# Performance work log

Hardware: AMD Instinct MI355X
Metric: run time of the kernel (lower is better)

The kernel has to match this reference:

```python
import jax, jax.numpy as jnp
import numpy as np

N = 100_000      # nodes
E = 1_600_000    # edges (avg degree 16)
IN, H, OUT = 128, 64, 32
G = 128          # graphs in batch
EPS = 1e-5


def setup_inputs() -> dict:
    key = jax.random.key(0)
    ks = jax.random.split(key, 12)
    x = jax.random.normal(ks[0], (N, IN), jnp.float32)
    edge_index = jax.random.randint(ks[1], (2, E), 0, N, dtype=jnp.int32)
    batch = jnp.sort(jax.random.randint(ks[2], (N,), 0, G, dtype=jnp.int32))
    # GCNConv weights (glorot-ish scaling), shared BatchNorm params, final linear
    W1 = jax.random.normal(ks[3], (IN, H), jnp.float32) / np.sqrt(IN)
    b1 = jnp.zeros((H,), jnp.float32)
    W2 = jax.random.normal(ks[4], (H, H), jnp.float32) / np.sqrt(H)
    b2 = jnp.zeros((H,), jnp.float32)
    gamma = jnp.ones((H,), jnp.float32)
    beta = jnp.zeros((H,), jnp.float32)
    linW = jax.random.normal(ks[5], (H, OUT), jnp.float32) / np.sqrt(H)
    linb = jnp.zeros((OUT,), jnp.float32)
    return dict(x=x, edge_index=edge_index, batch=batch, W1=W1, b1=b1,
                W2=W2, b2=b2, gamma=gamma, beta=beta, linW=linW, linb=linb)


def _gcn_edges(edge_index):
    # add self loops (PyG GCNConv default) and symmetric normalization
    loop = jnp.arange(N, dtype=edge_index.dtype)
    src = jnp.concatenate([edge_index[0], loop])
    dst = jnp.concatenate([edge_index[1], loop])
    deg = jax.ops.segment_sum(jnp.ones_like(src, jnp.float32), dst, num_segments=N)
    dis = jnp.where(deg > 0, jax.lax.rsqrt(deg), 0.0)
    norm = dis[src] * dis[dst]          # [E+N]
    return src, dst, norm


def _gcn_conv(h, W, b, src, dst, norm):
    h = h @ W                            # [N, out] small GEMM first (PyG order)
    msg = h[src] * norm[:, None]         # gather + edgewise normalize
    return jax.ops.segment_sum(msg, dst, num_segments=N) + b  # scatter-add


def _batchnorm(h, gamma, beta):
    # training-mode batch stats over nodes (biased variance, as torch BN)
    mean = h.mean(axis=0)
    var = jnp.mean((h - mean) ** 2, axis=0)
    return (h - mean) * jax.lax.rsqrt(var + EPS) * gamma + beta


def reference(x, edge_index, batch, W1, b1, W2, b2, gamma, beta, linW, linb):
    src, dst, norm = _gcn_edges(edge_index)
    h = jax.nn.relu(_batchnorm(_gcn_conv(x, W1, b1, src, dst, norm), gamma, beta))
    h = jax.nn.relu(_batchnorm(_gcn_conv(h, W2, b2, src, dst, norm), gamma, beta))
    # global mean pool over graph ids
    sums = jax.ops.segment_sum(h, batch, num_segments=G)
    cnts = jax.ops.segment_sum(jnp.ones((N,), h.dtype), batch, num_segments=G)
    pooled = sums / jnp.maximum(cnts, 1.0)[:, None]   # [G, H]
    return pooled @ linW + linb                        # [G, OUT]
```

## Files before the change

### kernel.cpp

```cpp
#include <hip/hip_runtime.h>

#define NNODES 100000
#define NEDGES 1600000
#define FIN 128
#define FH 64
#define FOUT 32
#define NGRAPH 128
#define EPSV 1e-5f

#define SCAN_BT 256
#define NBLK ((NNODES + SCAN_BT - 1) / SCAN_BT)
#define GM ((NNODES + 63) / 64)
#define FILLBLK 2048

typedef unsigned short ushort_t;
typedef __attribute__((ext_vector_type(8))) short bf16x8;
typedef __attribute__((ext_vector_type(4))) float f32x4;

__device__ inline unsigned f2bf(float f) {
  union { float f; unsigned u; } x;
  x.f = f;
  return (x.u + 0x7fffu + ((x.u >> 16) & 1u)) >> 16;
}
__device__ inline unsigned pack2(float a, float b) { return f2bf(a) | (f2bf(b) << 16); }
__device__ inline float bflo(unsigned u) {
  union { unsigned u; float f; } x;
  x.u = u << 16;
  return x.f;
}
__device__ inline float bfhi(unsigned u) {
  union { unsigned u; float f; } x;
  x.u = u & 0xffff0000u;
  return x.f;
}
__device__ inline float bfone(ushort_t v) {
  union { unsigned u; float f; } x;
  x.u = ((unsigned)v) << 16;
  return x.f;
}


__global__ void k_deg_accum(const int* __restrict__ dst, int* __restrict__ deg) {
  const int SLICE = NNODES / 8;
  int xcd = blockIdx.x & 7;
  int lo = xcd * SLICE, hi = lo + SLICE;
  int chunk = blockIdx.x >> 3;
  int nchunk = gridDim.x >> 3;
  for (int i = chunk * blockDim.x + threadIdx.x; i < NEDGES; i += nchunk * blockDim.x) {
    int d = dst[i];
    if (d >= lo && d < hi) atomicAdd(&deg[d], 1);
  }
}


__global__ void k_blocksum(const int* __restrict__ deg, int* __restrict__ bsum) {
  __shared__ int ls[SCAN_BT];
  int b = blockIdx.x, t = threadIdx.x;
  int i = b * SCAN_BT + t;
  ls[t] = (i < NNODES) ? deg[i] : 0;
  __syncthreads();
  for (int s = SCAN_BT / 2; s > 0; s >>= 1) {
    if (t < s) ls[t] += ls[t + s];
    __syncthreads();
  }
  if (t == 0) bsum[b] = ls[0];
}

__global__ void k_scan_bsums(const int* __restrict__ bsum, int* __restrict__ boff) {
  __shared__ int ls[512];
  int t = threadIdx.x;
  int v = (t < NBLK) ? bsum[t] : 0;
  ls[t] = v;
  __syncthreads();
  for (int s = 1; s < 512; s <<= 1) {
    int add = (t >= s) ? ls[t - s] : 0;
    __syncthreads();
    ls[t] += add;
    __syncthreads();
  }
  if (t < NBLK) boff[t] = ls[t] - v;
}

__global__ void k_scan_final(const int* __restrict__ deg, const int* __restrict__ boff,
                             int* __restrict__ off, float* __restrict__ dis) {
  __shared__ int ls[SCAN_BT];
  int b = blockIdx.x, t = threadIdx.x;
  int i = b * SCAN_BT + t;
  int v = (i < NNODES) ? deg[i] : 0;
  ls[t] = v;
  __syncthreads();
  for (int s = 1; s < SCAN_BT; s <<= 1) {
    int add = (t >= s) ? ls[t - s] : 0;
    __syncthreads();
    ls[t] += add;
    __syncthreads();
  }
  if (i < NNODES) {
    off[i] = boff[b] + ls[t] - v;
    dis[i] = rsqrtf((float)v + 1.0f);
  }
  if (i == NNODES - 1) off[NNODES] = boff[b] + ls[t];
}


template <int K, bool BN>
__device__ __forceinline__ void gemm_body(int bid, const void* __restrict__ Ap,
                                          const float* __restrict__ W,
                                          const float* __restrict__ stats,
                                          const float* __restrict__ gamma,
                                          const float* __restrict__ beta,
                                          const float* __restrict__ dis,
                                          ushort_t* __restrict__ out) {
  const int WT = K + 8;
  __shared__ ushort_t wt[64 * (K + 8)];
  __shared__ float bn_sc[K], bn_sh[K];
  if (BN && threadIdx.x < K) {
    int f = threadIdx.x;
    float mean = stats[f] * (1.0f / NNODES);
    float var = stats[K + f] * (1.0f / NNODES) - mean * mean;
    float s = gamma[f] * rsqrtf(var + EPSV);
    bn_sc[f] = s;
    bn_sh[f] = beta[f] - mean * s;
  }
  for (int idx = threadIdx.x; idx < K * 64; idx += 256) {
    int k = idx >> 6, col = idx & 63;
    wt[col * WT + k] = (ushort_t)f2bf(W[idx]);
  }
  __syncthreads();

  int wave = threadIdx.x >> 6;
  int lane = threadIdx.x & 63;
  int rrow = lane & 15;
  int g = lane >> 4;
  int row0 = (bid * 4 + wave) * 16;
  int arow = min(row0 + rrow, NNODES - 1);

  f32x4 acc0 = {0.f, 0.f, 0.f, 0.f}, acc1 = acc0, acc2 = acc0, acc3 = acc0;

#pragma unroll
  for (int ks = 0; ks < K / 32; ++ks) {
    int koff = ks * 32 + g * 8;
    float xs[8];
    if (BN) {
      const ushort_t* a = (const ushort_t*)Ap + (long long)arow * K;
      uint4 ua = *(const uint4*)(a + koff);
      xs[0] = bflo(ua.x); xs[1] = bfhi(ua.x);
      xs[2] = bflo(ua.y); xs[3] = bfhi(ua.y);
      xs[4] = bflo(ua.z); xs[5] = bfhi(ua.z);
      xs[6] = bflo(ua.w); xs[7] = bfhi(ua.w);
#pragma unroll
      for (int j = 0; j < 8; ++j)
        xs[j] = fmaxf(fmaf(xs[j], bn_sc[koff + j], bn_sh[koff + j]), 0.0f);
    } else {
      const float* a = (const float*)Ap + (long long)arow * K;
      f32x4 xa = __builtin_nontemporal_load((const f32x4*)(a + koff));
      f32x4 xb = __builtin_nontemporal_load((const f32x4*)(a + koff + 4));
      xs[0] = xa.x; xs[1] = xa.y; xs[2] = xa.z; xs[3] = xa.w;
      xs[4] = xb.x; xs[5] = xb.y; xs[6] = xb.z; xs[7] = xb.w;
    }
    bf16x8 af;
#pragma unroll
    for (int j = 0; j < 8; ++j) af[j] = (short)f2bf(xs[j]);
    bf16x8 b0 = *(const bf16x8*)&wt[(0 * 16 + rrow) * WT + koff];
    bf16x8 b1 = *(const bf16x8*)&wt[(1 * 16 + rrow) * WT + koff];
    bf16x8 b2 = *(const bf16x8*)&wt[(2 * 16 + rrow) * WT + koff];
    bf16x8 b3 = *(const bf16x8*)&wt[(3 * 16 + rrow) * WT + koff];
    acc0 = __builtin_amdgcn_mfma_f32_16x16x32_bf16(af, b0, acc0, 0, 0, 0);
    acc1 = __builtin_amdgcn_mfma_f32_16x16x32_bf16(af, b1, acc1, 0, 0, 0);
    acc2 = __builtin_amdgcn_mfma_f32_16x16x32_bf16(af, b2, acc2, 0, 0, 0);
    acc3 = __builtin_amdgcn_mfma_f32_16x16x32_bf16(af, b3, acc3, 0, 0, 0);
  }

  int orow0 = row0 + g * 4;
#pragma unroll
  for (int r = 0; r < 4; ++r) {
    int orow = orow0 + r;
    if (orow < NNODES) {
      float d = dis[orow];
      ushort_t* o = out + (long long)orow * FH + rrow;
      o[0] = (ushort_t)f2bf(acc0[r] * d);
      o[16] = (ushort_t)f2bf(acc1[r] * d);
      o[32] = (ushort_t)f2bf(acc2[r] * d);
      o[48] = (ushort_t)f2bf(acc3[r] * d);
    }
  }
}

template <int K, bool BN>
__global__ void k_gemm_mfma(const void* __restrict__ A, const float* __restrict__ W,
                            const float* __restrict__ stats, const float* __restrict__ gamma,
                            const float* __restrict__ beta, const float* __restrict__ dis,
                            ushort_t* __restrict__ out) {
  gemm_body<K, BN>(blockIdx.x, A, W, stats, gamma, beta, dis, out);
}


__global__ void k_fill_gemm1(const float* __restrict__ x, const float* __restrict__ W1,
                             const float* __restrict__ dis, ushort_t* __restrict__ bufA,
                             const int* __restrict__ src, const int* __restrict__ dst,
                             const int* __restrict__ off, int* __restrict__ cursor,
                             int* __restrict__ csr) {
  if (blockIdx.x < GM) {
    gemm_body<FIN, false>(blockIdx.x, x, W1, nullptr, nullptr, nullptr, dis, bufA);
  } else {
    int bb = blockIdx.x - GM;
    const int SLICE = NNODES / 8;
    int xcd = bb & 7;
    int lo = xcd * SLICE, hi = lo + SLICE;
    int chunk = bb >> 3;
    int nchunk = FILLBLK >> 3;
    for (int i = chunk * blockDim.x + threadIdx.x; i < NEDGES; i += nchunk * blockDim.x) {
      int d = dst[i];
      if (d >= lo && d < hi) {
        int p = atomicAdd(&cursor[d], 1);
        csr[off[d] + p] = src[i];
      }
    }
  }
}


#define ACC8(acc, u, ok)                       \
  acc[0] += (ok) ? bflo(u.x) : 0.0f;           \
  acc[1] += (ok) ? bfhi(u.x) : 0.0f;           \
  acc[2] += (ok) ? bflo(u.y) : 0.0f;           \
  acc[3] += (ok) ? bfhi(u.y) : 0.0f;           \
  acc[4] += (ok) ? bflo(u.z) : 0.0f;           \
  acc[5] += (ok) ? bfhi(u.z) : 0.0f;           \
  acc[6] += (ok) ? bflo(u.w) : 0.0f;           \
  acc[7] += (ok) ? bfhi(u.w) : 0.0f;

__global__ void k_gather(const ushort_t* __restrict__ hs, const int* __restrict__ csr,
                         const int* __restrict__ off, const float* __restrict__ dis,
                         ushort_t* __restrict__ out, float* __restrict__ stats) {
  __shared__ float ls[2 * FH];
  int tid = threadIdx.x;
  if (tid < 2 * FH) ls[tid] = 0.0f;
  __syncthreads();
  int lane = tid & 63;
  int q = lane >> 3;
  int i = lane & 7;
  int wid = (blockIdx.x * blockDim.x + tid) >> 6;
  int nw = (gridDim.x * blockDim.x) >> 6;
  const int HALF = NNODES / 2;
  float s1[8], s2[8];
#pragma unroll
  for (int f = 0; f < 8; ++f) s1[f] = s2[f] = 0.0f;

  for (int p = wid; p < HALF; p += nw) {
    int dA = p, dB = p + HALF;
    int bA = off[dA], eA = off[dA + 1];
    int bB = off[dB], eB = off[dB + 1];
    uint4 selfA = *(const uint4*)(hs + (long long)dA * FH + i * 8);
    uint4 selfB = *(const uint4*)(hs + (long long)dB * FH + i * 8);
    float accA[8], accB[8];
#pragma unroll
    for (int f = 0; f < 8; ++f) accA[f] = accB[f] = 0.0f;
    bool q0 = (q == 0);
    ACC8(accA, selfA, q0);
    ACC8(accB, selfB, q0);

    int nA = (eA - bA + 15) >> 4, nB = (eB - bB + 15) >> 4;
    int niter = max(nA, nB);
    int lastA = max(eA - 1, 0), lastB = max(eB - 1, 0);
    int kA0 = bA + q, kA1 = bA + q + 8;
    int kB0 = bB + q, kB1 = bB + q + 8;
    for (int j = 0; j < niter; ++j) {
      int a0 = kA0 + 16 * j, a1 = kA1 + 16 * j;
      int b0 = kB0 + 16 * j, b1 = kB1 + 16 * j;
      int cA0 = csr[min(a0, lastA)];
      int cA1 = csr[min(a1, lastA)];
      int cB0 = csr[min(b0, lastB)];
      int cB1 = csr[min(b1, lastB)];
      uint4 uA0 = *(const uint4*)(hs + (long long)cA0 * FH + i * 8);
      uint4 uA1 = *(const uint4*)(hs + (long long)cA1 * FH + i * 8);
      uint4 uB0 = *(const uint4*)(hs + (long long)cB0 * FH + i * 8);
      uint4 uB1 = *(const uint4*)(hs + (long long)cB1 * FH + i * 8);
      bool A0 = a0 < eA, A1 = a1 < eA, B0 = b0 < eB, B1 = b1 < eB;
      ACC8(accA, uA0, A0);
      ACC8(accA, uA1, A1);
      ACC8(accB, uB0, B0);
      ACC8(accB, uB1, B1);
    }
#pragma unroll
    for (int f = 0; f < 8; ++f) {
      accA[f] += __shfl_xor(accA[f], 8);
      accA[f] += __shfl_xor(accA[f], 16);
      accA[f] += __shfl_xor(accA[f], 32);
      accB[f] += __shfl_xor(accB[f], 8);
      accB[f] += __shfl_xor(accB[f], 16);
      accB[f] += __shfl_xor(accB[f], 32);
    }
    float ddA = dis[dA], ddB = dis[dB];
#pragma unroll
    for (int f = 0; f < 8; ++f) {
      accA[f] *= ddA;
      accB[f] *= ddB;
      s1[f] += accA[f] + accB[f];
      s2[f] += accA[f] * accA[f] + accB[f] * accB[f];
    }
    if (q == 0) {
      uint4 o;
      o.x = pack2(accA[0], accA[1]);
      o.y = pack2(accA[2], accA[3]);
      o.z = pack2(accA[4], accA[5]);
      o.w = pack2(accA[6], accA[7]);
      *(uint4*)(out + (long long)dA * FH + i * 8) = o;
    } else if (q == 1) {
      uint4 o;
      o.x = pack2(accB[0], accB[1]);
      o.y = pack2(accB[2], accB[3]);
      o.z = pack2(accB[4], accB[5]);
      o.w = pack2(accB[6], accB[7]);
      *(uint4*)(out + (long long)dB * FH + i * 8) = o;
    }
  }
  if (q == 2) {
#pragma unroll
    for (int f = 0; f < 8; ++f) {
      atomicAdd(&ls[i * 8 + f], s1[f]);
      atomicAdd(&ls[FH + i * 8 + f], s2[f]);
    }
  }
  __syncthreads();
  if (tid < 2 * FH) atomicAdd(&stats[tid], ls[tid]);
}


#define POOL_WAVES 1024

__global__ void k_pool(const ushort_t* __restrict__ h, const int* __restrict__ batch,
                       const float* __restrict__ stats, const float* __restrict__ gamma,
                       const float* __restrict__ beta, float* __restrict__ pooled,
                       float* __restrict__ cnt) {
  const int CHUNK = (NNODES + POOL_WAVES - 1) / POOL_WAVES;
  int lane = threadIdx.x & 63;
  int wid = (blockIdx.x * blockDim.x + threadIdx.x) >> 6;
  int start = wid * CHUNK;
  if (start >= NNODES) return;
  int end = min(start + CHUNK, NNODES);
  float mean = stats[lane] * (1.0f / NNODES);
  float var = stats[FH + lane] * (1.0f / NNODES) - mean * mean;
  float sc = gamma[lane] * rsqrtf(var + EPSV);
  float sh = beta[lane] - mean * sc;
  int cur = batch[start];
  float acc = 0.0f;
  int cl = 0;
  for (int n = start; n < end; ++n) {
    int g = batch[n];
    if (g != cur) {
      atomicAdd(&pooled[cur * FH + lane], acc);
      if (lane == 0) atomicAdd(&cnt[cur], (float)cl);
      acc = 0.0f;
      cl = 0;
      cur = g;
    }
    float v = fmaf(bfone(h[(long long)n * FH + lane]), sc, sh);
    acc += fmaxf(v, 0.0f);
    ++cl;
  }
  atomicAdd(&pooled[cur * FH + lane], acc);
  if (lane == 0) atomicAdd(&cnt[cur], (float)cl);
}


__global__ void k_final(const float* __restrict__ pooled, const float* __restrict__ cnt,
                        const float* __restrict__ linW, const float* __restrict__ linb,
                        float* __restrict__ out) {
  int t = blockIdx.x * blockDim.x + threadIdx.x;
  if (t >= NGRAPH * FOUT) return;
  int g = t / FOUT, o = t % FOUT;
  float inv = 1.0f / fmaxf(cnt[g], 1.0f);
  float acc = linb[o];
#pragma unroll
  for (int k = 0; k < FH; ++k) acc = fmaf(pooled[g * FH + k] * inv, linW[k * FOUT + o], acc);
  out[t] = acc;
}

extern "C" void kernel_launch(void* const* d_in, const int* in_sizes, int n_in,
                              void* d_out, int out_size, void* d_ws, size_t ws_size,
                              hipStream_t stream) {
  const float* x = (const float*)d_in[0];
  const int* edge_index = (const int*)d_in[1];
  const int* batch = (const int*)d_in[2];
  const float* W1 = (const float*)d_in[3];
  const float* W2 = (const float*)d_in[5];
  const float* gamma = (const float*)d_in[7];
  const float* beta = (const float*)d_in[8];
  const float* linW = (const float*)d_in[9];
  const float* linb = (const float*)d_in[10];
  float* out = (float*)d_out;

  const int* esrc = edge_index;
  const int* edst = edge_index + NEDGES;

  ushort_t* bufA = (ushort_t*)d_ws;
  ushort_t* bufB = bufA + (long long)NNODES * FH;
  float* dis = (float*)(bufB + (long long)NNODES * FH);
  int* off = (int*)(dis + NNODES);
  int* csr = off + (NNODES + 1);
  int* bsum = csr + NEDGES;
  int* boff = bsum + NBLK;
  int* deg = boff + NBLK;
  int* cursor = deg + NNODES;
  float* stats1 = (float*)(cursor + NNODES);
  float* stats2 = stats1 + 2 * FH;
  float* pooled = stats2 + 2 * FH;
  float* cnt = pooled + NGRAPH * FH;

  const int BT = 256;

  hipMemsetAsync(deg, 0,
                 (size_t)(2 * NNODES + 2 * 2 * FH + NGRAPH * FH + NGRAPH) * sizeof(int), stream);

  k_deg_accum<<<2048, BT, 0, stream>>>(edst, deg);
  k_blocksum<<<NBLK, SCAN_BT, 0, stream>>>(deg, bsum);
  k_scan_bsums<<<1, 512, 0, stream>>>(bsum, boff);
  k_scan_final<<<NBLK, SCAN_BT, 0, stream>>>(deg, boff, off, dis);
  k_fill_gemm1<<<GM + FILLBLK, BT, 0, stream>>>(x, W1, dis, bufA, esrc, edst, off, cursor, csr);

  k_gather<<<2048, BT, 0, stream>>>(bufA, csr, off, dis, bufB, stats1);

  k_gemm_mfma<FH, true><<<GM, BT, 0, stream>>>(bufB, W2, stats1, gamma, beta, dis, bufA);
  k_gather<<<2048, BT, 0, stream>>>(bufA, csr, off, dis, bufB, stats2);

  k_pool<<<POOL_WAVES * 64 / BT, BT, 0, stream>>>(bufB, batch, stats2, gamma, beta, pooled, cnt);
  k_final<<<(NGRAPH * FOUT + BT - 1) / BT, BT, 0, stream>>>(pooled, cnt, linW, linb, out);
}
```

Before: 425.1 us.

## Fuse all GCN stages into one cooperative persistent kernel with grid syncs

```diff
diff --git a/kernel.cpp b/kernel.cpp
--- a/kernel.cpp
+++ b/kernel.cpp
@@ -1,4 +1,7 @@
 #include <hip/hip_runtime.h>
+#include <hip/hip_cooperative_groups.h>
+
+namespace cg = cooperative_groups;
 
 #define NNODES 100000
 #define NEDGES 1600000
@@ -8,10 +11,11 @@
 #define NGRAPH 128
 #define EPSV 1e-5f
 
-#define SCAN_BT 256
-#define NBLK ((NNODES + SCAN_BT - 1) / SCAN_BT)
+#define NBLK ((NNODES + 255) / 256)
 #define GM ((NNODES + 63) / 64)
+#define FILLITEMS 1024
 #define FILLBLK 2048
+#define POOL_WAVES 1024
 
 typedef unsigned short ushort_t;
 typedef __attribute__((ext_vector_type(8))) short bf16x8;
@@ -39,68 +43,32 @@
   return x.f;
 }
 
-
-__global__ void k_deg_accum(const int* __restrict__ dst, int* __restrict__ deg) {
-  const int SLICE = NNODES / 8;
-  int xcd = blockIdx.x & 7;
-  int lo = xcd * SLICE, hi = lo + SLICE;
-  int chunk = blockIdx.x >> 3;
-  int nchunk = gridDim.x >> 3;
-  for (int i = chunk * blockDim.x + threadIdx.x; i < NEDGES; i += nchunk * blockDim.x) {
-    int d = dst[i];
-    if (d >= lo && d < hi) atomicAdd(&deg[d], 1);
-  }
-}
-
-
-__global__ void k_blocksum(const int* __restrict__ deg, int* __restrict__ bsum) {
-  __shared__ int ls[SCAN_BT];
-  int b = blockIdx.x, t = threadIdx.x;
-  int i = b * SCAN_BT + t;
-  ls[t] = (i < NNODES) ? deg[i] : 0;
-  __syncthreads();
-  for (int s = SCAN_BT / 2; s > 0; s >>= 1) {
-    if (t < s) ls[t] += ls[t + s];
-    __syncthreads();
-  }
-  if (t == 0) bsum[b] = ls[0];
-}
-
-__global__ void k_scan_bsums(const int* __restrict__ bsum, int* __restrict__ boff) {
-  __shared__ int ls[512];
-  int t = threadIdx.x;
-  int v = (t < NBLK) ? bsum[t] : 0;
-  ls[t] = v;
-  __syncthreads();
-  for (int s = 1; s < 512; s <<= 1) {
-    int add = (t >= s) ? ls[t - s] : 0;
-    __syncthreads();
-    ls[t] += add;
-    __syncthreads();
-  }
-  if (t < NBLK) boff[t] = ls[t] - v;
-}
-
-__global__ void k_scan_final(const int* __restrict__ deg, const int* __restrict__ boff,
-                             int* __restrict__ off, float* __restrict__ dis) {
-  __shared__ int ls[SCAN_BT];
-  int b = blockIdx.x, t = threadIdx.x;
-  int i = b * SCAN_BT + t;
-  int v = (i < NNODES) ? deg[i] : 0;
-  ls[t] = v;
-  __syncthreads();
-  for (int s = 1; s < SCAN_BT; s <<= 1) {
-    int add = (t >= s) ? ls[t - s] : 0;
-    __syncthreads();
-    ls[t] += add;
-    __syncthreads();
-  }
-  if (i < NNODES) {
-    off[i] = boff[b] + ls[t] - v;
-    dis[i] = rsqrtf((float)v + 1.0f);
-  }
-  if (i == NNODES - 1) off[NNODES] = boff[b] + ls[t];
-}
+struct P {
+  const float* x;
+  const int* src;
+  const int* dst;
+  const int* batch;
+  const float* W1;
+  const float* W2;
+  const float* gamma;
+  const float* beta;
+  const float* linW;
+  const float* linb;
+  float* out;
+  ushort_t* bufA;
+  ushort_t* bufB;
+  float* dis;
+  int* off;
+  int* csr;
+  int* bsum;
+  int* boff;
+  int* deg;
+  int* cursor;
+  float* stats1;
+  float* stats2;
+  float* pooled;
+  float* cnt;
+};
 
 
 template <int K, bool BN>
@@ -110,10 +78,10 @@
                                           const float* __restrict__ gamma,
                                           const float* __restrict__ beta,
                                           const float* __restrict__ dis,
-                                          ushort_t* __restrict__ out) {
+                                          ushort_t* __restrict__ out, ushort_t* wt,
+                                          float* bn_sc, float* bn_sh) {
   const int WT = K + 8;
-  __shared__ ushort_t wt[64 * (K + 8)];
-  __shared__ float bn_sc[K], bn_sh[K];
+  __syncthreads();
   if (BN && threadIdx.x < K) {
     int f = threadIdx.x;
     float mean = stats[f] * (1.0f / NNODES);
@@ -186,39 +154,6 @@
   }
 }
 
-template <int K, bool BN>
-__global__ void k_gemm_mfma(const void* __restrict__ A, const float* __restrict__ W,
-                            const float* __restrict__ stats, const float* __restrict__ gamma,
-                            const float* __restrict__ beta, const float* __restrict__ dis,
-                            ushort_t* __restrict__ out) {
-  gemm_body<K, BN>(blockIdx.x, A, W, stats, gamma, beta, dis, out);
-}
-
-
-__global__ void k_fill_gemm1(const float* __restrict__ x, const float* __restrict__ W1,
-                             const float* __restrict__ dis, ushort_t* __restrict__ bufA,
-                             const int* __restrict__ src, const int* __restrict__ dst,
-                             const int* __restrict__ off, int* __restrict__ cursor,
-                             int* __restrict__ csr) {
-  if (blockIdx.x < GM) {
-    gemm_body<FIN, false>(blockIdx.x, x, W1, nullptr, nullptr, nullptr, dis, bufA);
-  } else {
-    int bb = blockIdx.x - GM;
-    const int SLICE = NNODES / 8;
-    int xcd = bb & 7;
-    int lo = xcd * SLICE, hi = lo + SLICE;
-    int chunk = bb >> 3;
-    int nchunk = FILLBLK >> 3;
-    for (int i = chunk * blockDim.x + threadIdx.x; i < NEDGES; i += nchunk * blockDim.x) {
-      int d = dst[i];
-      if (d >= lo && d < hi) {
-        int p = atomicAdd(&cursor[d], 1);
-        csr[off[d] + p] = src[i];
-      }
-    }
-  }
-}
-
 
 #define ACC8(acc, u, ok)                       \
   acc[0] += (ok) ? bflo(u.x) : 0.0f;           \
@@ -230,25 +165,25 @@
   acc[6] += (ok) ? bflo(u.w) : 0.0f;           \
   acc[7] += (ok) ? bfhi(u.w) : 0.0f;
 
-__global__ void k_gather(const ushort_t* __restrict__ hs, const int* __restrict__ csr,
-                         const int* __restrict__ off, const float* __restrict__ dis,
-                         ushort_t* __restrict__ out, float* __restrict__ stats) {
-  __shared__ float ls[2 * FH];
+__device__ void gather_body(const ushort_t* __restrict__ hs, const int* __restrict__ csr,
+                            const int* __restrict__ off, const float* __restrict__ dis,
+                            ushort_t* __restrict__ out, float* __restrict__ stats,
+                            float* lsf, int nw) {
   int tid = threadIdx.x;
-  if (tid < 2 * FH) ls[tid] = 0.0f;
+  __syncthreads();
+  if (tid < 2 * FH) lsf[tid] = 0.0f;
   __syncthreads();
   int lane = tid & 63;
   int q = lane >> 3;
   int i = lane & 7;
-  int wid = (blockIdx.x * blockDim.x + tid) >> 6;
-  int nw = (gridDim.x * blockDim.x) >> 6;
+  int wid = (blockIdx.x * 256 + tid) >> 6;
   const int HALF = NNODES / 2;
   float s1[8], s2[8];
 #pragma unroll
   for (int f = 0; f < 8; ++f) s1[f] = s2[f] = 0.0f;
 
-  for (int p = wid; p < HALF; p += nw) {
-    int dA = p, dB = p + HALF;
+  for (int pnode = wid; pnode < HALF; pnode += nw) {
+    int dA = pnode, dB = pnode + HALF;
     int bA = off[dA], eA = off[dA + 1];
     int bB = off[dB], eB = off[dB + 1];
     uint4 selfA = *(const uint4*)(hs + (long long)dA * FH + i * 8);
@@ -318,16 +253,118 @@
   if (q == 2) {
 #pragma unroll
     for (int f = 0; f < 8; ++f) {
-      atomicAdd(&ls[i * 8 + f], s1[f]);
-      atomicAdd(&ls[FH + i * 8 + f], s2[f]);
-    }
-  }
-  __syncthreads();
-  if (tid < 2 * FH) atomicAdd(&stats[tid], ls[tid]);
-}
-
-
-#define POOL_WAVES 1024
+      atomicAdd(&lsf[i * 8 + f], s1[f]);
+      atomicAdd(&lsf[FH + i * 8 + f], s2[f]);
+    }
+  }
+  __syncthreads();
+  if (tid < 2 * FH) atomicAdd(&stats[tid], lsf[tid]);
+}
+
+
+__global__ void k_deg_accum(const int* __restrict__ dst, int* __restrict__ deg) {
+  const int SLICE = NNODES / 8;
+  int xcd = blockIdx.x & 7;
+  int lo = xcd * SLICE, hi = lo + SLICE;
+  int chunk = blockIdx.x >> 3;
+  int nchunk = gridDim.x >> 3;
+  for (int i = chunk * blockDim.x + threadIdx.x; i < NEDGES; i += nchunk * blockDim.x) {
+    int d = dst[i];
+    if (d >= lo && d < hi) atomicAdd(&deg[d], 1);
+  }
+}
+
+__global__ void k_blocksum(const int* __restrict__ deg, int* __restrict__ bsum) {
+  __shared__ int ls[256];
+  int b = blockIdx.x, t = threadIdx.x;
+  int i = b * 256 + t;
+  ls[t] = (i < NNODES) ? deg[i] : 0;
+  __syncthreads();
+  for (int s = 128; s > 0; s >>= 1) {
+    if (t < s) ls[t] += ls[t + s];
+    __syncthreads();
+  }
+  if (t == 0) bsum[b] = ls[0];
+}
+
+__global__ void k_scan_bsums(const int* __restrict__ bsum, int* __restrict__ boff) {
+  __shared__ int ls[512];
+  int t = threadIdx.x;
+  int v = (t < NBLK) ? bsum[t] : 0;
+  ls[t] = v;
+  __syncthreads();
+  for (int s = 1; s < 512; s <<= 1) {
+    int add = (t >= s) ? ls[t - s] : 0;
+    __syncthreads();
+    ls[t] += add;
+    __syncthreads();
+  }
+  if (t < NBLK) boff[t] = ls[t] - v;
+}
+
+__global__ void k_scan_final(const int* __restrict__ deg, const int* __restrict__ boff,
+                             int* __restrict__ off, float* __restrict__ dis) {
+  __shared__ int ls[256];
+  int b = blockIdx.x, t = threadIdx.x;
+  int i = b * 256 + t;
+  int v = (i < NNODES) ? deg[i] : 0;
+  ls[t] = v;
+  __syncthreads();
+  for (int s = 1; s < 256; s <<= 1) {
+    int add = (t >= s) ? ls[t - s] : 0;
+    __syncthreads();
+    ls[t] += add;
+    __syncthreads();
+  }
+  if (i < NNODES) {
+    off[i] = boff[b] + ls[t] - v;
+    dis[i] = rsqrtf((float)v + 1.0f);
+  }
+  if (i == NNODES - 1) off[NNODES] = boff[b] + ls[t];
+}
+
+__global__ void k_fill_gemm1(const float* __restrict__ x, const float* __restrict__ W1,
+                             const float* __restrict__ dis, ushort_t* __restrict__ bufA,
+                             const int* __restrict__ src, const int* __restrict__ dst,
+                             const int* __restrict__ off, int* __restrict__ cursor,
+                             int* __restrict__ csr) {
+  __shared__ ushort_t wt[64 * (FIN + 8)];
+  if (blockIdx.x < GM) {
+    gemm_body<FIN, false>(blockIdx.x, x, W1, nullptr, nullptr, nullptr, dis, bufA, wt,
+                          nullptr, nullptr);
+  } else {
+    int bb = blockIdx.x - GM;
+    const int SLICE = NNODES / 8;
+    int xcd = bb & 7;
+    int lo = xcd * SLICE, hi = lo + SLICE;
+    int chunk = bb >> 3;
+    int nchunk = FILLBLK >> 3;
+    for (int i = chunk * blockDim.x + threadIdx.x; i < NEDGES; i += nchunk * blockDim.x) {
+      int d = dst[i];
+      if (d >= lo && d < hi) {
+        int p = atomicAdd(&cursor[d], 1);
+        csr[off[d] + p] = src[i];
+      }
+    }
+  }
+}
+
+template <int K, bool BN>
+__global__ void k_gemm_mfma(const void* __restrict__ A, const float* __restrict__ W,
+                            const float* __restrict__ stats, const float* __restrict__ gamma,
+                            const float* __restrict__ beta, const float* __restrict__ dis,
+                            ushort_t* __restrict__ out) {
+  __shared__ ushort_t wt[64 * (K + 8)];
+  __shared__ float sc[K], sh[K];
+  gemm_body<K, BN>(blockIdx.x, A, W, stats, gamma, beta, dis, out, wt, sc, sh);
+}
+
+__global__ void k_gather(const ushort_t* __restrict__ hs, const int* __restrict__ csr,
+                         const int* __restrict__ off, const float* __restrict__ dis,
+                         ushort_t* __restrict__ out, float* __restrict__ stats) {
+  __shared__ float lsf[2 * FH];
+  gather_body(hs, csr, off, dis, out, stats, lsf, (gridDim.x * blockDim.x) >> 6);
+}
 
 __global__ void k_pool(const ushort_t* __restrict__ h, const int* __restrict__ batch,
                        const float* __restrict__ stats, const float* __restrict__ gamma,
@@ -363,7 +400,6 @@
   if (lane == 0) atomicAdd(&cnt[cur], (float)cl);
 }
 
-
 __global__ void k_final(const float* __restrict__ pooled, const float* __restrict__ cnt,
                         const float* __restrict__ linW, const float* __restrict__ linb,
                         float* __restrict__ out) {
@@ -377,53 +413,228 @@
   out[t] = acc;
 }
 
+
+__global__ __launch_bounds__(256, 4) void mega(P p) {
+  cg::grid_group grid = cg::this_grid();
+  __shared__ __align__(16) char smem[17920];
+  ushort_t* wt = (ushort_t*)smem;
+  float* bnsc = (float*)(smem + 17408);
+  float* bnsh = bnsc + FH;
+  int* lsi = (int*)smem;
+  float* lsf = (float*)smem;
+  int tid = threadIdx.x;
+  int nwv = gridDim.x * 4;
+
+  {
+    const int SLICE = NNODES / 8;
+    int xcd = blockIdx.x & 7;
+    int lo = xcd * SLICE, hi = lo + SLICE;
+    int chunk = blockIdx.x >> 3;
+    int nchunk = gridDim.x >> 3;
+    for (int i = chunk * 256 + tid; i < NEDGES; i += nchunk * 256) {
+      int d = p.dst[i];
+      if (d >= lo && d < hi) atomicAdd(&p.deg[d], 1);
+    }
+  }
+  __threadfence();
+  grid.sync();
+
+  if (blockIdx.x < NBLK) {
+    int i = blockIdx.x * 256 + tid;
+    lsi[tid] = (i < NNODES) ? p.deg[i] : 0;
+    __syncthreads();
+    for (int s = 128; s > 0; s >>= 1) {
+      if (tid < s) lsi[tid] += lsi[tid + s];
+      __syncthreads();
+    }
+    if (tid == 0) p.bsum[blockIdx.x] = lsi[0];
+  }
+  __threadfence();
+  grid.sync();
+
+  if (blockIdx.x == 0) {
+    int e0 = 2 * tid, e1 = 2 * tid + 1;
+    int b0 = (e0 < NBLK) ? p.bsum[e0] : 0;
+    int b1 = (e1 < NBLK) ? p.bsum[e1] : 0;
+    lsi[tid] = b0 + b1;
+    __syncthreads();
+    for (int s = 1; s < 256; s <<= 1) {
+      int add = (tid >= s) ? lsi[tid - s] : 0;
+      __syncthreads();
+      lsi[tid] += add;
+      __syncthreads();
+    }
+    int excl = lsi[tid] - (b0 + b1);
+    if (e0 < NBLK) p.boff[e0] = excl;
+    if (e1 < NBLK) p.boff[e1] = excl + b0;
+  }
+  __threadfence();
+  grid.sync();
+
+  if (blockIdx.x < NBLK) {
+    int b = blockIdx.x;
+    int i = b * 256 + tid;
+    int v = (i < NNODES) ? p.deg[i] : 0;
+    lsi[tid] = v;
+    __syncthreads();
+    for (int s = 1; s < 256; s <<= 1) {
+      int add = (tid >= s) ? lsi[tid - s] : 0;
+      __syncthreads();
+      lsi[tid] += add;
+      __syncthreads();
+    }
+    if (i < NNODES) {
+      p.off[i] = p.boff[b] + lsi[tid] - v;
+      p.dis[i] = rsqrtf((float)v + 1.0f);
+    }
+    if (i == NNODES - 1) p.off[NNODES] = p.boff[b] + lsi[tid];
+  }
+  __threadfence();
+  grid.sync();
+
+  for (int vb = blockIdx.x; vb < GM + FILLITEMS; vb += gridDim.x) {
+    if (vb < GM) {
+      gemm_body<FIN, false>(vb, p.x, p.W1, nullptr, nullptr, nullptr, p.dis, p.bufA, wt,
+                            bnsc, bnsh);
+    } else {
+      int it = vb - GM;
+      const int SLICE = NNODES / 8;
+      int cls = it & 7;
+      int lo = cls * SLICE, hi = lo + SLICE;
+      int chunk = it >> 3;
+      const int nch = FILLITEMS >> 3;
+      for (int i = chunk * 256 + tid; i < NEDGES; i += nch * 256) {
+        int d = p.dst[i];
+        if (d >= lo && d < hi) {
+          int pos = atomicAdd(&p.cursor[d], 1);
+          p.csr[p.off[d] + pos] = p.src[i];
+        }
+      }
+    }
+  }
+  __threadfence();
+  grid.sync();
+
+  gather_body(p.bufA, p.csr, p.off, p.dis, p.bufB, p.stats1, lsf, nwv);
+  __threadfence();
+  grid.sync();
+
+  for (int vb = blockIdx.x; vb < GM; vb += gridDim.x)
+    gemm_body<FH, true>(vb, p.bufB, p.W2, p.stats1, p.gamma, p.beta, p.dis, p.bufA, wt,
+                        bnsc, bnsh);
+  __threadfence();
+  grid.sync();
+
+  gather_body(p.bufA, p.csr, p.off, p.dis, p.bufB, p.stats2, lsf, nwv);
+  __threadfence();
+  grid.sync();
+
+  {
+    const int CHUNK = (NNODES + nwv - 1) / nwv;
+    int lane = tid & 63;
+    int wid = blockIdx.x * 4 + (tid >> 6);
+    int start = wid * CHUNK;
+    if (start < NNODES) {
+      int end = min(start + CHUNK, NNODES);
+      float mean = p.stats2[lane] * (1.0f / NNODES);
+      float var = p.stats2[FH + lane] * (1.0f / NNODES) - mean * mean;
+      float sc = p.gamma[lane] * rsqrtf(var + EPSV);
+      float sh = p.beta[lane] - mean * sc;
+      int cur = p.batch[start];
+      float acc = 0.0f;
+      int cl = 0;
+      for (int n = start; n < end; ++n) {
+        int g = p.batch[n];
+        if (g != cur) {
+          atomicAdd(&p.pooled[cur * FH + lane], acc);
+          if (lane == 0) atomicAdd(&p.cnt[cur], (float)cl);
+          acc = 0.0f;
+          cl = 0;
+          cur = g;
+        }
+        float v = fmaf(bfone(p.bufB[(long long)n * FH + lane]), sc, sh);
+        acc += fmaxf(v, 0.0f);
+        ++cl;
+      }
+      atomicAdd(&p.pooled[cur * FH + lane], acc);
+      if (lane == 0) atomicAdd(&p.cnt[cur], (float)cl);
+    }
+  }
+  __threadfence();
+  grid.sync();
+
+  for (int t = blockIdx.x * 256 + tid; t < NGRAPH * FOUT; t += gridDim.x * 256) {
+    int g = t / FOUT, o = t % FOUT;
+    float inv = 1.0f / fmaxf(p.cnt[g], 1.0f);
+    float acc = p.linb[o];
+#pragma unroll
+    for (int k = 0; k < FH; ++k)
+      acc = fmaf(p.pooled[g * FH + k] * inv, p.linW[k * FOUT + o], acc);
+    p.out[t] = acc;
+  }
+}
+
 extern "C" void kernel_launch(void* const* d_in, const int* in_sizes, int n_in,
                               void* d_out, int out_size, void* d_ws, size_t ws_size,
                               hipStream_t stream) {
-  const float* x = (const float*)d_in[0];
-  const int* edge_index = (const int*)d_in[1];
-  const int* batch = (const int*)d_in[2];
-  const float* W1 = (const float*)d_in[3];
-  const float* W2 = (const float*)d_in[5];
-  const float* gamma = (const float*)d_in[7];
-  const float* beta = (const float*)d_in[8];
-  const float* linW = (const float*)d_in[9];
-  const float* linb = (const float*)d_in[10];
-  float* out = (float*)d_out;
-
-  const int* esrc = edge_index;
-  const int* edst = edge_index + NEDGES;
-
-  ushort_t* bufA = (ushort_t*)d_ws;
-  ushort_t* bufB = bufA + (long long)NNODES * FH;
-  float* dis = (float*)(bufB + (long long)NNODES * FH);
-  int* off = (int*)(dis + NNODES);
-  int* csr = off + (NNODES + 1);
-  int* bsum = csr + NEDGES;
-  int* boff = bsum + NBLK;
-  int* deg = boff + NBLK;
-  int* cursor = deg + NNODES;
-  float* stats1 = (float*)(cursor + NNODES);
-  float* stats2 = stats1 + 2 * FH;
-  float* pooled = stats2 + 2 * FH;
-  float* cnt = pooled + NGRAPH * FH;
-
-  const int BT = 256;
-
-  hipMemsetAsync(deg, 0,
-                 (size_t)(2 * NNODES + 2 * 2 * FH + NGRAPH * FH + NGRAPH) * sizeof(int), stream);
-
-  k_deg_accum<<<2048, BT, 0, stream>>>(edst, deg);
-  k_blocksum<<<NBLK, SCAN_BT, 0, stream>>>(deg, bsum);
-  k_scan_bsums<<<1, 512, 0, stream>>>(bsum, boff);
-  k_scan_final<<<NBLK, SCAN_BT, 0, stream>>>(deg, boff, off, dis);
-  k_fill_gemm1<<<GM + FILLBLK, BT, 0, stream>>>(x, W1, dis, bufA, esrc, edst, off, cursor, csr);
-
-  k_gather<<<2048, BT, 0, stream>>>(bufA, csr, off, dis, bufB, stats1);
-
-  k_gemm_mfma<FH, true><<<GM, BT, 0, stream>>>(bufB, W2, stats1, gamma, beta, dis, bufA);
-  k_gather<<<2048, BT, 0, stream>>>(bufA, csr, off, dis, bufB, stats2);
-
-  k_pool<<<POOL_WAVES * 64 / BT, BT, 0, stream>>>(bufB, batch, stats2, gamma, beta, pooled, cnt);
-  k_final<<<(NGRAPH * FOUT + BT - 1) / BT, BT, 0, stream>>>(pooled, cnt, linW, linb, out);
-}
+  P p;
+  p.x = (const float*)d_in[0];
+  p.src = (const int*)d_in[1];
+  p.dst = (const int*)d_in[1] + NEDGES;
+  p.batch = (const int*)d_in[2];
+  p.W1 = (const float*)d_in[3];
+  p.W2 = (const float*)d_in[5];
+  p.gamma = (const float*)d_in[7];
+  p.beta = (const float*)d_in[8];
+  p.linW = (const float*)d_in[9];
+  p.linb = (const float*)d_in[10];
+  p.out = (float*)d_out;
+
+  p.bufA = (ushort_t*)d_ws;
+  p.bufB = p.bufA + (long long)NNODES * FH;
+  p.dis = (float*)(p.bufB + (long long)NNODES * FH);
+  p.off = (int*)(p.dis + NNODES);
+  p.csr = p.off + (NNODES + 1);
+  p.bsum = p.csr + NEDGES;
+  p.boff = p.bsum + NBLK;
+  p.deg = p.boff + NBLK;
+  p.cursor = p.deg + NNODES;
+  p.stats1 = (float*)(p.cursor + NNODES);
+  p.stats2 = p.stats1 + 2 * FH;
+  p.pooled = p.stats2 + 2 * FH;
+  p.cnt = p.pooled + NGRAPH * FH;
+
+  (void)hipMemsetAsync(p.deg, 0,
+                       (size_t)(2 * NNODES + 2 * 2 * FH + NGRAPH * FH + NGRAPH) * sizeof(int),
+                       stream);
+
+  int nb = 0;
+  hipError_t oerr =
+      hipOccupancyMaxActiveBlocksPerMultiprocessor(&nb, (const void*)mega, 256, 0);
+  hipError_t lerr = hipErrorUnknown;
+  if (oerr == hipSuccess && nb > 0) {
+    int gridn = nb * 256;
+    if (gridn > 1024) gridn = 1024;
+    gridn &= ~7;
+    if (gridn >= 512) {
+      void* args[] = {&p};
+      lerr = hipLaunchCooperativeKernel((void*)mega, dim3(gridn), dim3(256), args, 0, stream);
+    }
+  }
+  if (lerr != hipSuccess) {
+    k_deg_accum<<<2048, 256, 0, stream>>>(p.dst, p.deg);
+    k_blocksum<<<NBLK, 256, 0, stream>>>(p.deg, p.bsum);
+    k_scan_bsums<<<1, 512, 0, stream>>>(p.bsum, p.boff);
+    k_scan_final<<<NBLK, 256, 0, stream>>>(p.deg, p.boff, p.off, p.dis);
+    k_fill_gemm1<<<GM + FILLBLK, 256, 0, stream>>>(p.x, p.W1, p.dis, p.bufA, p.src, p.dst,
+                                                   p.off, p.cursor, p.csr);
+    k_gather<<<2048, 256, 0, stream>>>(p.bufA, p.csr, p.off, p.dis, p.bufB, p.stats1);
+    k_gemm_mfma<FH, true><<<GM, 256, 0, stream>>>(p.bufB, p.W2, p.stats1, p.gamma, p.beta,
+                                                  p.dis, p.bufA);
+    k_gather<<<2048, 256, 0, stream>>>(p.bufA, p.csr, p.off, p.dis, p.bufB, p.stats2);
+    k_pool<<<POOL_WAVES * 64 / 256, 256, 0, stream>>>(p.bufB, p.batch, p.stats2, p.gamma,
+                                                      p.beta, p.pooled, p.cnt);
+    k_final<<<(NGRAPH * FOUT + 255) / 256, 256, 0, stream>>>(p.pooled, p.cnt, p.linW, p.linb,
+                                                             p.out);
+  }
+}
```

Result: slower. 1.272 ms (+199.2%).
